# Kernel optimization log

Measured on AMD Instinct MI355X. Metric: run time of the kernel, lower is better.

The kernel has to match this reference:

```python
import jax, jax.numpy as jnp
import numpy as np

IMG_SIZE = 640
NUM_CLASSES = 80
KA = 3
STRIDES = (8, 16, 32)
CONF_THRESH = 0.001
NMS_THRESH = 0.6
ANCHORS = np.array([[12, 16], [19, 36], [40, 28],
                    [36, 75], [76, 55], [72, 146],
                    [142, 110], [192, 243], [459, 401]], np.float32).reshape(3, 3, 2)
CLS_OFFSET = 4.0  # > max normalized coord (1.0); separates classes for class-wise NMS


def _make_grid(stride):
    f = IMG_SIZE // stride
    gy, gx = jnp.meshgrid(jnp.arange(f), jnp.arange(f), indexing='ij')
    # [HW, 1, 2] in (x, y) order, row-major over (H, W) like permute(1,2,0).view(-1,...)
    return jnp.stack([gx, gy], axis=-1).reshape(-1, 1, 2).astype(jnp.float32)


def _decode_level(pred, level):
    # pred: [KA*(1+C+4), H, W] -> obj [HW*KA,1], cls [HW*KA,C], boxes [HW*KA,4]
    C = NUM_CLASSES
    p = jnp.transpose(pred, (1, 2, 0)).reshape(-1, KA * (1 + C + 4))  # [HW, ch]
    obj = p[:, :KA].reshape(-1, 1)
    cls = p[:, KA:KA * (1 + C)].reshape(-1, C)
    reg = p[:, KA * (1 + C):].reshape(-1, KA, 4)
    grid = _make_grid(STRIDES[level])               # [HW, 1, 2]
    anchors = jnp.asarray(ANCHORS[level])           # [KA, 2]
    xy = (jax.nn.sigmoid(reg[..., :2]) + grid) * STRIDES[level]
    wh = jnp.exp(reg[..., 2:]) * anchors
    box = jnp.concatenate([xy - wh * 0.5, xy + wh * 0.5], axis=-1).reshape(-1, 4)
    return obj, cls, box


def _greedy_nms(boxes, scores, valid, thresh):
    # Faithful sequential greedy NMS (same math as the numpy loop), via lax.scan.
    N = boxes.shape[0]
    order = jnp.argsort(-scores)
    b = boxes[order]
    v = valid[order]
    areas = (b[:, 2] - b[:, 0]) * (b[:, 3] - b[:, 1])
    idx = jnp.arange(N)

    def step(suppressed, i):
        keep_i = v[i] & jnp.logical_not(suppressed[i])
        xx1 = jnp.maximum(b[i, 0], b[:, 0])
        yy1 = jnp.maximum(b[i, 1], b[:, 1])
        xx2 = jnp.minimum(b[i, 2], b[:, 2])
        yy2 = jnp.minimum(b[i, 3], b[:, 3])
        w = jnp.maximum(1e-28, xx2 - xx1)
        h = jnp.maximum(1e-28, yy2 - yy1)
        inter = w * h
        ovr = inter / (areas[i] + areas - inter + 1e-14)
        suppressed = suppressed | (keep_i & (ovr > thresh) & (idx > i))
        return suppressed, keep_i

    _, kept_sorted = jax.lax.scan(step, jnp.zeros(N, bool), idx)
    return jnp.zeros(N, bool).at[order].set(kept_sorted)


def _forward(pred_s, pred_m, pred_l):
    outs = [_decode_level(p, i) for i, p in enumerate((pred_s, pred_m, pred_l))]
    obj = jnp.concatenate([o[0] for o in outs], axis=0)   # [N, 1]
    cls = jnp.concatenate([o[1] for o in outs], axis=0)   # [N, C]
    box = jnp.concatenate([o[2] for o in outs], axis=0)   # [N, 4]
    bboxes = jnp.clip(box / IMG_SIZE, 0.0, 1.0)
    scores = jax.nn.sigmoid(obj) * jax.nn.softmax(cls, axis=-1)  # [N, C]
    cls_inds = jnp.argmax(scores, axis=1)
    conf = jnp.max(scores, axis=1)
    valid = conf >= CONF_THRESH
    # per-class NMS == class-offset trick: different classes never overlap
    nms_boxes = bboxes + cls_inds.astype(bboxes.dtype)[:, None] * CLS_OFFSET
    keep = _greedy_nms(jax.lax.stop_gradient(nms_boxes),
                       jax.lax.stop_gradient(conf), valid, NMS_THRESH)
    return bboxes, conf, cls_inds, keep


def setup_inputs() -> dict:
    key = jax.random.key(0)
    k1, k2, k3 = jax.random.split(key, 3)
    ch = KA * (1 + NUM_CLASSES + 4)  # 255
    return {
        'pred_s': jax.random.normal(k1, (ch, 80, 80), jnp.float32),
        'pred_m': jax.random.normal(k2, (ch, 40, 40), jnp.float32),
        'pred_l': jax.random.normal(k3, (ch, 20, 20), jnp.float32),
    }


def reference(pred_s, pred_m, pred_l):
    # returns fixed-shape (bboxes [N,4], scores [N], cls_inds [N], keep mask [N])
    return _forward(pred_s, pred_m, pred_l)
```

## Files before the change

### kernel.cpp

```cpp
#include <hip/hip_runtime.h>

typedef unsigned long long u64;
typedef unsigned int u32;

#define NCLS 80
#define CAP 512
#define ST_STRIDE 36

__device__ __constant__ float c_AW[9] = {12.f,19.f,40.f,36.f,76.f,72.f,142.f,192.f,459.f};
__device__ __constant__ float c_AH[9] = {16.f,36.f,28.f,75.f,55.f,146.f,110.f,243.f,401.f};

__global__ __launch_bounds__(128)
void decode_kernel(const float* __restrict__ p0,
                   const float* __restrict__ p1,
                   const float* __restrict__ p2,
                   float* __restrict__ out)
{
    const int bid = blockIdx.x;
    const float* p; int f, strd, base, lvl, rem;
    if (bid < 600)      { p = p0; f = 80; strd = 8;  base = 0;     lvl = 0; rem = bid; }
    else if (bid < 750) { p = p1; f = 40; strd = 16; base = 19200; lvl = 1; rem = bid - 600; }
    else                { p = p2; f = 20; strd = 32; base = 24000; lvl = 2; rem = bid - 750; }
    const int a    = rem % 3;
    const int tile = rem / 3;
    const int HW   = f * f;
    const int hw0  = tile << 5;

    __shared__ float st[88][ST_STRIDE];

    const int tid = threadIdx.x;

    {
        const int col = tid & 31;
        const int r0  = tid >> 5;
        const int hp  = min(hw0 + col, HW - 1);
        float vals[22];
        #pragma unroll
        for (int k = 0; k < 22; ++k) {
            const int row = r0 + 4 * k;
            if (row < 85) {
                const int ch = (row == 0) ? a
                             : (row <= 80 ? (3 + 80 * a + (row - 1))
                                          : (243 + 4 * a + (row - 81)));
                vals[k] = p[ch * HW + hp];
            }
        }
        #pragma unroll
        for (int k = 0; k < 22; ++k) {
            const int row = r0 + 4 * k;
            if (row < 85) st[row][col] = vals[k];
        }
    }
    __syncthreads();

    const int g = tid >> 2, q = tid & 3;
    const int cell = hw0 + g;
    if (cell >= HW) return;
    const int gx = cell % f;
    const int gy = cell / f;

    float v[20];
    #pragma unroll
    for (int k = 0; k < 20; ++k) v[k] = st[1 + 4 * k + q][g];

    float lmax = v[0];
    #pragma unroll
    for (int k = 1; k < 20; ++k) lmax = fmaxf(lmax, v[k]);
    float gm = lmax;
    gm = fmaxf(gm, __shfl_xor(gm, 1));
    gm = fmaxf(gm, __shfl_xor(gm, 2));

    float ls = 0.f, bp = -1.f; int ba_ = 0;
    #pragma unroll
    for (int k = 0; k < 20; ++k) {
        float pc = expf(v[k] - gm);
        ls += pc;
        if (pc > bp) { bp = pc; ba_ = 4 * k + q; }
    }
    float gs = ls;
    gs += __shfl_xor(gs, 1);
    gs += __shfl_xor(gs, 2);
    {
        float bp2 = __shfl_xor(bp, 1); int ba2 = __shfl_xor(ba_, 1);
        if (bp2 > bp || (bp2 == bp && ba2 < ba_)) { bp = bp2; ba_ = ba2; }
        bp2 = __shfl_xor(bp, 2); ba2 = __shfl_xor(ba_, 2);
        if (bp2 > bp || (bp2 == bp && ba2 < ba_)) { bp = bp2; ba_ = ba2; }
    }

    if (q != 0) return;

    float obj = st[0][g];
    float tx = st[81][g];
    float ty = st[82][g];
    float tw = st[83][g];
    float th = st[84][g];

    float sig  = 1.f / (1.f + expf(-obj));
    float conf = sig * (bp / gs);
    const int n = base + cell * 3 + a;

    float sx = 1.f / (1.f + expf(-tx));
    float sy = 1.f / (1.f + expf(-ty));
    float cx = (sx + (float)gx) * (float)strd;
    float cy = (sy + (float)gy) * (float)strd;
    const int ai = lvl * 3 + a;
    float w  = expf(tw) * c_AW[ai];
    float h  = expf(th) * c_AH[ai];
    float hx = w * 0.5f, hy = h * 0.5f;
    float x1 = (cx - hx) / 640.0f;
    float y1 = (cy - hy) / 640.0f;
    float x2 = (cx + hx) / 640.0f;
    float y2 = (cy + hy) / 640.0f;
    x1 = fminf(fmaxf(x1, 0.f), 1.f);
    y1 = fminf(fmaxf(y1, 0.f), 1.f);
    x2 = fminf(fmaxf(x2, 0.f), 1.f);
    y2 = fminf(fmaxf(y2, 0.f), 1.f);

    *(float4*)(out + n * 4) = make_float4(x1, y1, x2, y2);
    out[100800 + n] = conf;
    out[126000 + n] = (float)ba_;
    out[151200 + n] = 0.0f;
}

__global__ __launch_bounds__(1024)
void nms_kernel(const float* __restrict__ out,
                float* __restrict__ out_keep)
{
    const int c = blockIdx.x;
    const int tid = threadIdx.x;
    const int wave = tid >> 6, lane = tid & 63;

    __shared__ int    scnt;
    __shared__ u64    skey[CAP];
    __shared__ float4 sbox[CAP + 1];
    __shared__ int    sgi[CAP];
    __shared__ u64    maskT[8 * CAP];

    if (tid == 0) scnt = 0;
    __syncthreads();

    const float* confp = out + 100800;
    const float* clsp  = out + 126000;
    for (int ib = tid; ib < 6300; ib += 1024) {
        const float4 cf4 = *(const float4*)(confp + ib * 4);
        const float4 cl4 = *(const float4*)(clsp  + ib * 4);
        #pragma unroll
        for (int k = 0; k < 4; ++k) {
            const float cf = (k == 0) ? cf4.x : (k == 1) ? cf4.y : (k == 2) ? cf4.z : cf4.w;
            const float cl = (k == 0) ? cl4.x : (k == 1) ? cl4.y : (k == 2) ? cl4.z : cl4.w;
            if ((int)cl == c && cf >= 0.001f) {
                const int i = ib * 4 + k;
                const int pos = atomicAdd(&scnt, 1);
                if (pos < CAP)
                    skey[pos] = ((u64)__float_as_uint(cf) << 32) | (u64)(~(u32)i);
            }
        }
    }
    __syncthreads();
    const int M  = min(scnt, CAP);
    const int MW = (M + 63) >> 6;

    if (wave < MW) {
        const int e = (wave << 6) + lane;
        if (e < M) {
            const u64 ke = skey[e];
            int rank = 0;
            int j = 0;
            for (; j + 8 <= M; j += 8) {
                rank += (int)(skey[j]   > ke) + (int)(skey[j+1] > ke)
                      + (int)(skey[j+2] > ke) + (int)(skey[j+3] > ke)
                      + (int)(skey[j+4] > ke) + (int)(skey[j+5] > ke)
                      + (int)(skey[j+6] > ke) + (int)(skey[j+7] > ke);
            }
            for (; j < M; ++j) rank += (int)(skey[j] > ke);

            const u32 gi = ~(u32)ke;
            const float4 b = *(const float4*)(out + gi * 4);
            const float off = 4.0f * (float)c;
            sbox[rank] = make_float4(b.x + off, b.y + off, b.z + off, b.w + off);
            sgi[rank]  = (int)gi;
        }
    }
    __syncthreads();

    const int ntiles = (MW * (MW + 1)) >> 1;
    for (int t = wave; t < ntiles; t += 16) {
        int rw = 0, acc = 0;
        while (t >= acc + (MW - rw)) { acc += MW - rw; ++rw; }
        const int cw = rw + (t - acc);
        const int j  = (cw << 6) + lane;
        const float4 cb = sbox[min(j, M - 1)];
        const float  ca = (cb.z - cb.x) * (cb.w - cb.y);
        const int r0 = rw << 6;
        const int r1 = min(r0 + 64, M);
        u64 bits = 0ull;
        float4 nb = sbox[r0];
        for (int i = r0; i < r1; ++i) {
            const float4 rb = nb;
            nb = sbox[i + 1];
            const float ra = (rb.z - rb.x) * (rb.w - rb.y);
            float xx1 = fmaxf(rb.x, cb.x);
            float yy1 = fmaxf(rb.y, cb.y);
            float xx2 = fminf(rb.z, cb.z);
            float yy2 = fminf(rb.w, cb.w);
            float ww = fmaxf(1e-28f, xx2 - xx1);
            float hh = fmaxf(1e-28f, yy2 - yy1);
            float inter = ww * hh;
            float ovr = inter / (ra + ca - inter + 1e-14f);
            bits |= (u64)((i < j) && (ovr >= 0.6f)) << (i & 63);
        }
        maskT[rw * CAP + j] = bits;
    }
    __syncthreads();

    if (wave != 0) return;

    u64 k0 = 0, k1 = 0, k2 = 0, k3 = 0, k4 = 0, k5 = 0, k6 = 0, k7 = 0;
    (void)k7;
#define MT(W) maskT[(W) * CAP + j]
#define TILE(W, PRE)                                                    \
    if ((W) < MW) {                                                     \
        const int j = ((W) << 6) + lane;                                \
        const u64 mine = MT(W);                                         \
        const u64 pre = (PRE);                                          \
        const int rm = M - ((W) << 6);                                  \
        const u64 valid = (rm >= 64) ? ~0ull : ((1ull << rm) - 1ull);   \
        u64 cand = valid & ~__ballot(pre != 0ull);                      \
        u64 kept = 0ull;                                                \
        while (cand) {                                                  \
            const u64 remv = cand & __ballot((mine & kept) != 0ull);    \
            cand &= ~remv;                                              \
            const u64 newk = cand & __ballot((mine & cand) == 0ull);    \
            kept |= newk;                                               \
            cand &= ~newk;                                              \
        }                                                               \
        k##W = kept;                                                    \
        if ((kept >> lane) & 1ull) out_keep[sgi[j]] = 1.0f;             \
    }
    TILE(0, 0ull)
    TILE(1, (MT(0)&k0))
    TILE(2, (MT(0)&k0)|(MT(1)&k1))
    TILE(3, (MT(0)&k0)|(MT(1)&k1)|(MT(2)&k2))
    TILE(4, (MT(0)&k0)|(MT(1)&k1)|(MT(2)&k2)|(MT(3)&k3))
    TILE(5, (MT(0)&k0)|(MT(1)&k1)|(MT(2)&k2)|(MT(3)&k3)|(MT(4)&k4))
    TILE(6, (MT(0)&k0)|(MT(1)&k1)|(MT(2)&k2)|(MT(3)&k3)|(MT(4)&k4)|(MT(5)&k5))
    TILE(7, (MT(0)&k0)|(MT(1)&k1)|(MT(2)&k2)|(MT(3)&k3)|(MT(4)&k4)|(MT(5)&k5)|(MT(6)&k6))
#undef TILE
#undef MT
}

extern "C" void kernel_launch(void* const* d_in, const int* in_sizes, int n_in,
                              void* d_out, int out_size, void* d_ws, size_t ws_size,
                              hipStream_t stream) {
    const float* p0 = (const float*)d_in[0];
    const float* p1 = (const float*)d_in[1];
    const float* p2 = (const float*)d_in[2];
    float* out = (float*)d_out;

    decode_kernel<<<789, 128, 0, stream>>>(p0, p1, p2, out);
    nms_kernel<<<NCLS, 1024, 0, stream>>>(out, out + 151200);
}
```

Before: 44.55 us.

## Decode with 8 lanes per anchor directly from global and wave-aggregate NMS compaction

The decode kernel drops the shared-memory transpose tile. It now assigns 8 threads per anchor, each reading 10 class logits straight from global memory with strided loads, reduced by 3-level shuffles. In the NMS gather phase, per-element shared atomics are replaced with ballot/popcount wave-aggregated compaction, so there is one atomic per wave per iteration. The decode change trades coalesced staging for more threads, and its loads are only partially coalesced because adjacent anchors alternate between channel groups.

```diff
diff --git a/kernel.cpp b/kernel.cpp
--- a/kernel.cpp
+++ b/kernel.cpp
@@ -3,101 +3,85 @@
 typedef unsigned long long u64;
 typedef unsigned int u32;
 
+#define N_TOT 25200
 #define NCLS 80
 #define CAP 512
-#define ST_STRIDE 36
 
 __device__ __constant__ float c_AW[9] = {12.f,19.f,40.f,36.f,76.f,72.f,142.f,192.f,459.f};
 __device__ __constant__ float c_AH[9] = {16.f,36.f,28.f,75.f,55.f,146.f,110.f,243.f,401.f};
 
-__global__ __launch_bounds__(128)
+__global__ __launch_bounds__(256)
 void decode_kernel(const float* __restrict__ p0,
                    const float* __restrict__ p1,
                    const float* __restrict__ p2,
                    float* __restrict__ out)
 {
-    const int bid = blockIdx.x;
-    const float* p; int f, strd, base, lvl, rem;
-    if (bid < 600)      { p = p0; f = 80; strd = 8;  base = 0;     lvl = 0; rem = bid; }
-    else if (bid < 750) { p = p1; f = 40; strd = 16; base = 19200; lvl = 1; rem = bid - 600; }
-    else                { p = p2; f = 20; strd = 32; base = 24000; lvl = 2; rem = bid - 750; }
-    const int a    = rem % 3;
-    const int tile = rem / 3;
-    const int HW   = f * f;
-    const int hw0  = tile << 5;
-
-    __shared__ float st[88][ST_STRIDE];
-
-    const int tid = threadIdx.x;
-
-    {
-        const int col = tid & 31;
-        const int r0  = tid >> 5;
-        const int hp  = min(hw0 + col, HW - 1);
-        float vals[22];
-        #pragma unroll
-        for (int k = 0; k < 22; ++k) {
-            const int row = r0 + 4 * k;
-            if (row < 85) {
-                const int ch = (row == 0) ? a
-                             : (row <= 80 ? (3 + 80 * a + (row - 1))
-                                          : (243 + 4 * a + (row - 81)));
-                vals[k] = p[ch * HW + hp];
-            }
-        }
-        #pragma unroll
-        for (int k = 0; k < 22; ++k) {
-            const int row = r0 + 4 * k;
-            if (row < 85) st[row][col] = vals[k];
-        }
-    }
-    __syncthreads();
-
-    const int g = tid >> 2, q = tid & 3;
-    const int cell = hw0 + g;
-    if (cell >= HW) return;
-    const int gx = cell % f;
-    const int gy = cell / f;
-
-    float v[20];
+    const int t = blockIdx.x * 256 + threadIdx.x;
+    const int n = t >> 3;
+    const int q = t & 7;
+    if (n >= N_TOT) return;
+
+    const float* p; int f, strd, base, lvl;
+    if (n < 19200)      { p = p0; f = 80; strd = 8;  base = 0;     lvl = 0; }
+    else if (n < 24000) { p = p1; f = 40; strd = 16; base = 19200; lvl = 1; }
+    else                { p = p2; f = 20; strd = 32; base = 24000; lvl = 2; }
+
+    const int r  = n - base;
+    const int hw = r / 3;
+    const int a  = r - hw * 3;
+    const int HW = f * f;
+    const int gx = hw % f;
+    const int gy = hw / f;
+    const float* cell = p + hw;
+    const float* clsp = cell + (3 + a * NCLS) * HW;
+
+    float obj = 0.f, tx = 0.f, ty = 0.f, tw = 0.f, th = 0.f;
+    if (q == 0) {
+        obj = cell[a * HW];
+        const float* regp = cell + (243 + a * 4) * HW;
+        tx = regp[0];
+        ty = regp[HW];
+        tw = regp[2 * HW];
+        th = regp[3 * HW];
+    }
+
+    float v[10];
     #pragma unroll
-    for (int k = 0; k < 20; ++k) v[k] = st[1 + 4 * k + q][g];
+    for (int k = 0; k < 10; ++k) v[k] = clsp[(8 * k + q) * HW];
 
     float lmax = v[0];
     #pragma unroll
-    for (int k = 1; k < 20; ++k) lmax = fmaxf(lmax, v[k]);
+    for (int k = 1; k < 10; ++k) lmax = fmaxf(lmax, v[k]);
     float gm = lmax;
     gm = fmaxf(gm, __shfl_xor(gm, 1));
     gm = fmaxf(gm, __shfl_xor(gm, 2));
+    gm = fmaxf(gm, __shfl_xor(gm, 4));
 
     float ls = 0.f, bp = -1.f; int ba_ = 0;
     #pragma unroll
-    for (int k = 0; k < 20; ++k) {
+    for (int k = 0; k < 10; ++k) {
         float pc = expf(v[k] - gm);
         ls += pc;
-        if (pc > bp) { bp = pc; ba_ = 4 * k + q; }
+        if (pc > bp) { bp = pc; ba_ = 8 * k + q; }
     }
     float gs = ls;
     gs += __shfl_xor(gs, 1);
     gs += __shfl_xor(gs, 2);
+    gs += __shfl_xor(gs, 4);
     {
-        float bp2 = __shfl_xor(bp, 1); int ba2 = __shfl_xor(ba_, 1);
+        float bp2; int ba2;
+        bp2 = __shfl_xor(bp, 1); ba2 = __shfl_xor(ba_, 1);
         if (bp2 > bp || (bp2 == bp && ba2 < ba_)) { bp = bp2; ba_ = ba2; }
         bp2 = __shfl_xor(bp, 2); ba2 = __shfl_xor(ba_, 2);
         if (bp2 > bp || (bp2 == bp && ba2 < ba_)) { bp = bp2; ba_ = ba2; }
+        bp2 = __shfl_xor(bp, 4); ba2 = __shfl_xor(ba_, 4);
+        if (bp2 > bp || (bp2 == bp && ba2 < ba_)) { bp = bp2; ba_ = ba2; }
     }
 
     if (q != 0) return;
-
-    float obj = st[0][g];
-    float tx = st[81][g];
-    float ty = st[82][g];
-    float tw = st[83][g];
-    float th = st[84][g];
 
     float sig  = 1.f / (1.f + expf(-obj));
     float conf = sig * (bp / gs);
-    const int n = base + cell * 3 + a;
 
     float sx = 1.f / (1.f + expf(-tx));
     float sy = 1.f / (1.f + expf(-ty));
@@ -141,19 +125,37 @@
 
     const float* confp = out + 100800;
     const float* clsp  = out + 126000;
-    for (int ib = tid; ib < 6300; ib += 1024) {
-        const float4 cf4 = *(const float4*)(confp + ib * 4);
-        const float4 cl4 = *(const float4*)(clsp  + ib * 4);
-        #pragma unroll
-        for (int k = 0; k < 4; ++k) {
-            const float cf = (k == 0) ? cf4.x : (k == 1) ? cf4.y : (k == 2) ? cf4.z : cf4.w;
-            const float cl = (k == 0) ? cl4.x : (k == 1) ? cl4.y : (k == 2) ? cl4.z : cl4.w;
-            if ((int)cl == c && cf >= 0.001f) {
-                const int i = ib * 4 + k;
-                const int pos = atomicAdd(&scnt, 1);
-                if (pos < CAP)
-                    skey[pos] = ((u64)__float_as_uint(cf) << 32) | (u64)(~(u32)i);
-            }
+    const u64 lt = (1ull << lane) - 1ull;
+    for (int itr = 0; itr < 7; ++itr) {
+        const int ib = itr * 1024 + tid;
+        const bool inb = (ib < 6300);
+        float4 cf4 = make_float4(-1.f, -1.f, -1.f, -1.f);
+        float4 cl4 = make_float4(0.f, 0.f, 0.f, 0.f);
+        if (inb) {
+            cf4 = *(const float4*)(confp + ib * 4);
+            cl4 = *(const float4*)(clsp  + ib * 4);
+        }
+        const bool m0 = inb && ((int)cl4.x == c) && (cf4.x >= 0.001f);
+        const bool m1 = inb && ((int)cl4.y == c) && (cf4.y >= 0.001f);
+        const bool m2 = inb && ((int)cl4.z == c) && (cf4.z >= 0.001f);
+        const bool m3 = inb && ((int)cl4.w == c) && (cf4.w >= 0.001f);
+        const u64 b0 = __ballot(m0), b1 = __ballot(m1), b2 = __ballot(m2), b3 = __ballot(m3);
+        const int t0 = __popcll(b0), t1 = __popcll(b1), t2 = __popcll(b2), t3 = __popcll(b3);
+        const int tot = t0 + t1 + t2 + t3;
+        int base = 0;
+        if (tot) {
+            if (lane == 0) base = atomicAdd(&scnt, tot);
+            base = __shfl(base, 0);
+            const int i0 = itr * 4096 + tid * 4;
+            int pos;
+            if (m0) { pos = base + __popcll(b0 & lt);
+                      if (pos < CAP) skey[pos] = ((u64)__float_as_uint(cf4.x) << 32) | (u64)(~(u32)(i0)); }
+            if (m1) { pos = base + t0 + __popcll(b1 & lt);
+                      if (pos < CAP) skey[pos] = ((u64)__float_as_uint(cf4.y) << 32) | (u64)(~(u32)(i0 + 1)); }
+            if (m2) { pos = base + t0 + t1 + __popcll(b2 & lt);
+                      if (pos < CAP) skey[pos] = ((u64)__float_as_uint(cf4.z) << 32) | (u64)(~(u32)(i0 + 2)); }
+            if (m3) { pos = base + t0 + t1 + t2 + __popcll(b3 & lt);
+                      if (pos < CAP) skey[pos] = ((u64)__float_as_uint(cf4.w) << 32) | (u64)(~(u32)(i0 + 3)); }
         }
     }
     __syncthreads();
@@ -257,6 +259,6 @@
     const float* p2 = (const float*)d_in[2];
     float* out = (float*)d_out;
 
-    decode_kernel<<<789, 128, 0, stream>>>(p0, p1, p2, out);
+    decode_kernel<<<(N_TOT * 8 + 255) / 256, 256, 0, stream>>>(p0, p1, p2, out);
     nms_kernel<<<NCLS, 1024, 0, stream>>>(out, out + 151200);
 }
```

Result: slower. 47.16 us (+5.9%).
